# Kernel optimization log

Hardware: AMD Instinct MI355X
Metric: run time of the kernel (lower is better)

The kernel has to match this reference:

```python
import jax, jax.numpy as jnp
import numpy as np

N_NODES = 50000
N_EDGES = 800000
D = 128
SAME_W = 0.3
CROSS_W = 1.0


def setup_inputs() -> dict:
    key = jax.random.key(0)
    k1, k2, k3, k4, k5 = jax.random.split(key, 5)
    x = jax.random.normal(k1, (N_NODES, D), dtype=jnp.float32)
    edge_index = jax.random.randint(k2, (2, N_EDGES), 0, N_NODES, dtype=jnp.int64)
    edge_weight = jax.random.uniform(k3, (N_EDGES,), dtype=jnp.float32)
    Wr1 = jax.random.normal(k4, (D, D), dtype=jnp.float32) * (1.0 / np.sqrt(D))
    Wr2 = jax.random.normal(k5, (D, D), dtype=jnp.float32) * (1.0 / np.sqrt(D))
    return {"x": x, "edge_index": edge_index, "edge_weight": edge_weight,
            "Wr1": Wr1, "Wr2": Wr2, "cell_len": 20000}


def _node_types(idx, cell_len):
    # get_node_types: type 0 if idx <= cell_len, else 1 (note the <=, faithful to source)
    return (idx > cell_len).astype(jnp.int32)


def _conv_layer(x, src, dst, per_edge_w, Wr, n_nodes):
    # gather -> weight -> scatter-mean -> + root linear
    msg = x[src] * per_edge_w[:, None]                       # [E, D]
    agg = jax.ops.segment_sum(msg, dst, num_segments=n_nodes)  # [N, D]
    cnt = jax.ops.segment_sum(jnp.ones_like(per_edge_w), dst, num_segments=n_nodes)
    agg = agg / jnp.maximum(cnt, 1.0)[:, None]               # mean aggr (0 if no edges)
    return agg + x @ Wr.T                                     # lin_r, bias=False


def reference(x, edge_index, edge_weight, Wr1, Wr2, cell_len):
    src, dst = edge_index[0], edge_index[1]
    same = _node_types(src, cell_len) == _node_types(dst, cell_len)
    type_w = jnp.where(same, SAME_W, CROSS_W).astype(x.dtype)
    w = type_w * edge_weight                                  # [E]
    n_nodes = x.shape[0]
    h = _conv_layer(x, src, dst, w, Wr1, n_nodes)
    out = _conv_layer(h, src, dst, w, Wr2, n_nodes)
    return out
```

## Files before the change

kernel.cpp:

```cpp
#include <hip/hip_runtime.h>
#include <cstdint>
#include <cstddef>

#define D 128
#define SAME_W 0.3f
#define CROSS_W 1.0f
#define NSLICE 8
#define EPT 8
#define CAP 64
#define GEMM_BLOCKS 512

using bf16x8 = __attribute__((ext_vector_type(8))) __bf16;
using f32x4  = __attribute__((ext_vector_type(4))) float;

__device__ __forceinline__ unsigned bf16rne(float f) {
    unsigned u = __float_as_uint(f);
    return (u + 0x7FFFu + ((u >> 16) & 1u)) >> 16;
}

__global__ __launch_bounds__(256) void k_pre(
    const int* __restrict__ src, const int* __restrict__ dst,
    const float* __restrict__ ew, const int* __restrict__ cell_len,
    int* __restrict__ cnt, unsigned* __restrict__ meta, int E, int sliceLen,
    int nFill,
    const float4* __restrict__ x4, uint2* __restrict__ xh2,
    uint2* __restrict__ xl2, unsigned* __restrict__ xq, int nvec, int nSplit,
    const float* __restrict__ W1, const float* __restrict__ W2,
    unsigned* __restrict__ wsh, unsigned* __restrict__ w12h,
    unsigned* __restrict__ w12l)
{
    const int b = blockIdx.x;
    if (b < nFill) {
        const int slice = b & (NSLICE - 1);
        const int lo = slice * sliceLen, hi = lo + sliceLen;
        const int base = (b >> 3) * (256 * EPT) + threadIdx.x;
        const int c = *cell_len;
        #pragma unroll
        for (int u = 0; u < EPT; ++u) {
            int e = base + u * 256;
            if (e < E) {
                int d = __builtin_nontemporal_load(&dst[e]);
                if (d >= lo && d < hi) {
                    int s = __builtin_nontemporal_load(&src[e]);
                    float w = __builtin_nontemporal_load(&ew[e]);
                    float wt = w * (((s > c) == (d > c)) ? SAME_W : CROSS_W);
                    int pos = atomicAdd(&cnt[d], 1);
                    if (pos < CAP)
                        meta[d * CAP + pos] = (unsigned)s | (bf16rne(wt) << 16);
                }
            }
        }
    } else if (b < nFill + nSplit) {
        int i = (b - nFill) * 256 + threadIdx.x;
        if (i >= nvec) return;
        float4 v = x4[i];
        unsigned h0 = bf16rne(v.x), h1 = bf16rne(v.y),
                 h2 = bf16rne(v.z), h3 = bf16rne(v.w);
        xh2[i] = make_uint2(h0 | (h1 << 16), h2 | (h3 << 16));
        float r0 = v.x - __uint_as_float(h0 << 16);
        float r1 = v.y - __uint_as_float(h1 << 16);
        float r2 = v.z - __uint_as_float(h2 << 16);
        float r3 = v.w - __uint_as_float(h3 << 16);
        xl2[i] = make_uint2(bf16rne(r0) | (bf16rne(r1) << 16),
                            bf16rne(r2) | (bf16rne(r3) << 16));
        int q = __builtin_amdgcn_cvt_pk_fp8_f32(v.x, v.y, 0, false);
        q = __builtin_amdgcn_cvt_pk_fp8_f32(v.z, v.w, q, true);
        xq[i] = (unsigned)q;
    } else {
        int t = (b - nFill - nSplit) * 256 + threadIdx.x;
        int j = t >> 6, kp = t & 63;
        int k0 = kp * 2;
        float d0 = 0.f, d1 = 0.f;
        #pragma unroll 4
        for (int m = 0; m < D; ++m) {
            float a = W2[j * D + m];
            d0 = fmaf(a, W1[m * D + k0], d0);
            d1 = fmaf(a, W1[m * D + k0 + 1], d1);
        }
        float s0 = W1[j * D + k0] + W2[j * D + k0];
        float s1 = W1[j * D + k0 + 1] + W2[j * D + k0 + 1];
        wsh[j * 64 + kp] = bf16rne(s0) | (bf16rne(s1) << 16);
        unsigned h0 = bf16rne(d0), h1 = bf16rne(d1);
        w12h[j * 64 + kp] = h0 | (h1 << 16);
        float r0 = d0 - __uint_as_float(h0 << 16);
        float r1 = d1 - __uint_as_float(h1 << 16);
        w12l[j * 64 + kp] = bf16rne(r0) | (bf16rne(r1) << 16);
    }
}

template <bool EMIT_FP8>
__global__ __launch_bounds__(256) void k_agg_fp8(const unsigned short* __restrict__ xq,
                                                 const uint4* __restrict__ meta4,
                                                 const int* __restrict__ cnt,
                                                 unsigned* __restrict__ outb,
                                                 unsigned short* __restrict__ outq,
                                                 int N) {
    int gid = blockIdx.x * blockDim.x + threadIdx.x;
    int node = gid >> 6;
    int lane = gid & 63;
    if (node >= N) return;
    const int cn0 = cnt[node];
    const int cn = min(cn0, CAP);
    const uint4* mrow = meta4 + (size_t)node * (CAP / 4);
    float ax0 = 0.f, ay0 = 0.f, ax1 = 0.f, ay1 = 0.f;
    int i = 0;
    #pragma unroll 1
    for (; i + 16 <= cn; i += 16) {
        uint4 mq[4];
        #pragma unroll
        for (int u = 0; u < 4; ++u) mq[u] = mrow[(i >> 2) + u];
        unsigned short v[16];
        #pragma unroll
        for (int u = 0; u < 16; ++u) {
            unsigned m = ((const unsigned*)mq)[u];
            v[u] = xq[(size_t)(m & 0xFFFFu) * 64 + lane];
        }
        #pragma unroll
        for (int u = 0; u < 16; ++u) {
            unsigned m = ((const unsigned*)mq)[u];
            float wt = __uint_as_float(m & 0xFFFF0000u);
            float vx = __builtin_amdgcn_cvt_f32_fp8((unsigned)v[u], 0);
            float vy = __builtin_amdgcn_cvt_f32_fp8((unsigned)v[u], 1);
            if (u & 1) { ax1 = fmaf(vx, wt, ax1); ay1 = fmaf(vy, wt, ay1); }
            else       { ax0 = fmaf(vx, wt, ax0); ay0 = fmaf(vy, wt, ay0); }
        }
    }
    #pragma unroll 1
    for (; i + 4 <= cn; i += 4) {
        uint4 mq = mrow[i >> 2];
        unsigned short v[4];
        #pragma unroll
        for (int u = 0; u < 4; ++u)
            v[u] = xq[(size_t)(((const unsigned*)&mq)[u] & 0xFFFFu) * 64 + lane];
        #pragma unroll
        for (int u = 0; u < 4; ++u) {
            unsigned m = ((const unsigned*)&mq)[u];
            float wt = __uint_as_float(m & 0xFFFF0000u);
            float vx = __builtin_amdgcn_cvt_f32_fp8((unsigned)v[u], 0);
            float vy = __builtin_amdgcn_cvt_f32_fp8((unsigned)v[u], 1);
            if (u & 1) { ax1 = fmaf(vx, wt, ax1); ay1 = fmaf(vy, wt, ay1); }
            else       { ax0 = fmaf(vx, wt, ax0); ay0 = fmaf(vy, wt, ay0); }
        }
    }
    for (; i < cn; ++i) {
        unsigned m = ((const unsigned*)mrow)[i];
        float wt = __uint_as_float(m & 0xFFFF0000u);
        unsigned short v = xq[(size_t)(m & 0xFFFFu) * 64 + lane];
        ax0 = fmaf(__builtin_amdgcn_cvt_f32_fp8((unsigned)v, 0), wt, ax0);
        ay0 = fmaf(__builtin_amdgcn_cvt_f32_fp8((unsigned)v, 1), wt, ay0);
    }
    const float scale = 1.0f / (float)max(cn0, 1);
    const float rx = (ax0 + ax1) * scale, ry = (ay0 + ay1) * scale;
    outb[(size_t)node * 64 + lane] = bf16rne(rx) | (bf16rne(ry) << 16);
    if (EMIT_FP8) {
        int q = __builtin_amdgcn_cvt_pk_fp8_f32(rx, ry, 0, false);
        outq[(size_t)node * 64 + lane] = (unsigned short)(q & 0xFFFF);
    }
}

__global__ __launch_bounds__(256, 2) void k_gemm2(
    const uint4* __restrict__ xh4, const uint4* __restrict__ xl4,
    const uint4* __restrict__ a1h4,
    const uint4* __restrict__ w12h4, const uint4* __restrict__ w12l4,
    const uint4* __restrict__ wsh4,
    const unsigned* __restrict__ a2b,
    float* __restrict__ fout, int N, int nTiles)
{
    const int t = threadIdx.x;
    const int wave = t >> 6, lane = t & 63;
    const int j0 = wave * 32;
    const int lr = lane & 15;
    const int q  = lane >> 4;

    union FU { uint4 u; bf16x8 v; };

    FU wA[2][4], wB[2][4], wC[2][4];
    #pragma unroll
    for (int jt = 0; jt < 2; ++jt) {
        const int brow = (j0 + jt * 16 + lr) * 16 + q;
        #pragma unroll
        for (int ks = 0; ks < 4; ++ks) {
            wA[jt][ks].u = w12h4[brow + ks * 4];
            wB[jt][ks].u = w12l4[brow + ks * 4];
            wC[jt][ks].u = wsh4[brow + ks * 4];
        }
    }

#define LOAD_TILE(BX, BL, BA, BC, TILE) do {                                   \
    int row_ = (TILE) * 16 + lr; if (row_ > N - 1) row_ = N - 1;               \
    const int ar_ = row_ * 16 + q;                                             \
    _Pragma("unroll")                                                          \
    for (int ks = 0; ks < 4; ++ks) {                                           \
        BX[ks].u = xh4[ar_ + ks * 4];                                          \
        BL[ks].u = xl4[ar_ + ks * 4];                                          \
        BA[ks].u = a1h4[ar_ + ks * 4];                                         \
    }                                                                          \
    _Pragma("unroll")                                                          \
    for (int jt = 0; jt < 2; ++jt)                                             \
        _Pragma("unroll")                                                      \
        for (int r = 0; r < 4; ++r) {                                          \
            int rr_ = (TILE) * 16 + q * 4 + r; if (rr_ > N - 1) rr_ = N - 1;   \
            BC[jt * 4 + r] = a2b[(size_t)rr_ * 64 + ((j0 + jt * 16 + lr) >> 1)]; \
        }                                                                      \
} while (0)

#define COMPUTE_STORE(BX, BL, BA, BC, TILE) do {                               \
    f32x4 c_[2];                                                               \
    c_[0] = (f32x4){0.f, 0.f, 0.f, 0.f};                                       \
    c_[1] = (f32x4){0.f, 0.f, 0.f, 0.f};                                       \
    _Pragma("unroll")                                                          \
    for (int jt = 0; jt < 2; ++jt)                                             \
        _Pragma("unroll")                                                      \
        for (int ks = 0; ks < 4; ++ks) {                                       \
            c_[jt] = __builtin_amdgcn_mfma_f32_16x16x32_bf16(BX[ks].v, wA[jt][ks].v, c_[jt], 0, 0, 0); \
            c_[jt] = __builtin_amdgcn_mfma_f32_16x16x32_bf16(BL[ks].v, wA[jt][ks].v, c_[jt], 0, 0, 0); \
            c_[jt] = __builtin_amdgcn_mfma_f32_16x16x32_bf16(BX[ks].v, wB[jt][ks].v, c_[jt], 0, 0, 0); \
            c_[jt] = __builtin_amdgcn_mfma_f32_16x16x32_bf16(BA[ks].v, wC[jt][ks].v, c_[jt], 0, 0, 0); \
        }                                                                      \
    _Pragma("unroll")                                                          \
    for (int jt = 0; jt < 2; ++jt)                                             \
        _Pragma("unroll")                                                      \
        for (int r = 0; r < 4; ++r) {                                          \
            int rr_ = (TILE) * 16 + q * 4 + r;                                 \
            if (rr_ < N) {                                                     \
                unsigned w_ = BC[jt * 4 + r];                                  \
                float ci_ = __uint_as_float((lr & 1) ? (w_ & 0xFFFF0000u) : (w_ << 16)); \
                fout[(size_t)rr_ * D + j0 + jt * 16 + lr] = c_[jt][r] + ci_;   \
            }                                                                  \
        }                                                                      \
} while (0)

    FU Axh[4], Axl[4], Aa1[4]; unsigned Aci[8];
    FU Bxh[4], Bxl[4], Ba1[4]; unsigned Bci[8];

    int tile = blockIdx.x;
    const int step = gridDim.x;
    if (tile >= nTiles) return;
    LOAD_TILE(Axh, Axl, Aa1, Aci, tile);
    while (true) {
        int tn = tile + step;
        if (tn < nTiles) LOAD_TILE(Bxh, Bxl, Ba1, Bci, tn);
        COMPUTE_STORE(Axh, Axl, Aa1, Aci, tile);
        tile = tn;
        if (tile >= nTiles) break;
        tn = tile + step;
        if (tn < nTiles) LOAD_TILE(Axh, Axl, Aa1, Aci, tn);
        COMPUTE_STORE(Bxh, Bxl, Ba1, Bci, tile);
        tile = tn;
        if (tile >= nTiles) break;
    }
#undef LOAD_TILE
#undef COMPUTE_STORE
}

extern "C" void kernel_launch(void* const* d_in, const int* in_sizes, int n_in,
                              void* d_out, int out_size, void* d_ws, size_t ws_size,
                              hipStream_t stream) {
    const float* x        = (const float*)d_in[0];
    const int*   ei       = (const int*)d_in[1];
    const float* ew       = (const float*)d_in[2];
    const float* Wr1      = (const float*)d_in[3];
    const float* Wr2      = (const float*)d_in[4];
    const int*   cell_len = (const int*)d_in[5];

    const int N = in_sizes[0] / D;
    const int E = in_sizes[1] / 2;
    const int* src = ei;
    const int* dst = ei + E;

    char* ws = (char*)d_ws;
    size_t off = 0;
    unsigned* meta = (unsigned*)(ws + off); off += (size_t)4 * CAP * N;
    int*      cnt  = (int*)     (ws + off); off += (size_t)4 * N;
    off = (off + 255) & ~(size_t)255;
    unsigned* xh   = (unsigned*)(ws + off); off += (size_t)2 * N * D;
    unsigned* xl   = (unsigned*)(ws + off); off += (size_t)2 * N * D;
    unsigned* a1h  = (unsigned*)(ws + off); off += (size_t)2 * N * D;
    unsigned* a2b  = (unsigned*)(ws + off); off += (size_t)2 * N * D;
    unsigned* xq   = (unsigned*)(ws + off); off += (size_t)1 * N * D;
    unsigned* a1q  = (unsigned*)(ws + off); off += (size_t)1 * N * D;
    unsigned* wsh  = (unsigned*)(ws + off); off += (size_t)2 * D * D;
    unsigned* w12h = (unsigned*)(ws + off); off += (size_t)2 * D * D;
    unsigned* w12l = (unsigned*)(ws + off); off += (size_t)2 * D * D;
    if (ws_size < off) return;
    float* out = (float*)d_out;

    hipMemsetAsync(cnt, 0, (size_t)4 * N, stream);

    const int sliceLen = (N + NSLICE - 1) / NSLICE;
    const int nFill  = ((E + 256 * EPT - 1) / (256 * EPT)) * NSLICE;
    const int xvec   = N * D / 4;
    const int nSplit = (xvec + 255) / 256;
    const int nW     = (D * 64 + 255) / 256;
    const int aggBlocks = (N + 3) / 4;
    const int nTiles = (N + 15) / 16;

    k_pre<<<nFill + nSplit + nW, 256, 0, stream>>>(
        src, dst, ew, cell_len, cnt, meta, E, sliceLen, nFill,
        (const float4*)x, (uint2*)xh, (uint2*)xl, xq, xvec, nSplit,
        Wr1, Wr2, wsh, w12h, w12l);

    k_agg_fp8<true ><<<aggBlocks, 256, 0, stream>>>(
        (const unsigned short*)xq, (const uint4*)meta, cnt,
        a1h, (unsigned short*)a1q, N);
    k_agg_fp8<false><<<aggBlocks, 256, 0, stream>>>(
        (const unsigned short*)a1q, (const uint4*)meta, cnt,
        a2b, nullptr, N);

    k_gemm2<<<GEMM_BLOCKS, 256, 0, stream>>>((const uint4*)xh, (const uint4*)xl,
                                             (const uint4*)a1h,
                                             (const uint4*)w12h, (const uint4*)w12l,
                                             (const uint4*)wsh, a2b, out, N, nTiles);
}
```

Measured before the change: 224.4 us.

## Split x to bf16 hi/lo inside GEMM instead of materializing in preprocessing

```diff
diff --git a/kernel.cpp b/kernel.cpp
--- a/kernel.cpp
+++ b/kernel.cpp
@@ -6,16 +6,39 @@
 #define SAME_W 0.3f
 #define CROSS_W 1.0f
 #define NSLICE 8
-#define EPT 8
 #define CAP 64
 #define GEMM_BLOCKS 512
 
 using bf16x8 = __attribute__((ext_vector_type(8))) __bf16;
 using f32x4  = __attribute__((ext_vector_type(4))) float;
+using i32x4  = __attribute__((ext_vector_type(4))) int;
+using u32x4  = __attribute__((ext_vector_type(4))) unsigned;
 
 __device__ __forceinline__ unsigned bf16rne(float f) {
     unsigned u = __float_as_uint(f);
     return (u + 0x7FFFu + ((u >> 16) & 1u)) >> 16;
+}
+
+__device__ __forceinline__ void cvt8(const float4 a, const float4 b,
+                                     uint4& hi, uint4& lo) {
+    unsigned h0 = bf16rne(a.x), h1 = bf16rne(a.y),
+             h2 = bf16rne(a.z), h3 = bf16rne(a.w);
+    unsigned h4 = bf16rne(b.x), h5 = bf16rne(b.y),
+             h6 = bf16rne(b.z), h7 = bf16rne(b.w);
+    hi.x = h0 | (h1 << 16); hi.y = h2 | (h3 << 16);
+    hi.z = h4 | (h5 << 16); hi.w = h6 | (h7 << 16);
+    float r0 = a.x - __uint_as_float(h0 << 16);
+    float r1 = a.y - __uint_as_float(h1 << 16);
+    float r2 = a.z - __uint_as_float(h2 << 16);
+    float r3 = a.w - __uint_as_float(h3 << 16);
+    float r4 = b.x - __uint_as_float(h4 << 16);
+    float r5 = b.y - __uint_as_float(h5 << 16);
+    float r6 = b.z - __uint_as_float(h6 << 16);
+    float r7 = b.w - __uint_as_float(h7 << 16);
+    lo.x = bf16rne(r0) | (bf16rne(r1) << 16);
+    lo.y = bf16rne(r2) | (bf16rne(r3) << 16);
+    lo.z = bf16rne(r4) | (bf16rne(r5) << 16);
+    lo.w = bf16rne(r6) | (bf16rne(r7) << 16);
 }
 
 __global__ __launch_bounds__(256) void k_pre(
@@ -23,8 +46,7 @@
     const float* __restrict__ ew, const int* __restrict__ cell_len,
     int* __restrict__ cnt, unsigned* __restrict__ meta, int E, int sliceLen,
     int nFill,
-    const float4* __restrict__ x4, uint2* __restrict__ xh2,
-    uint2* __restrict__ xl2, unsigned* __restrict__ xq, int nvec, int nSplit,
+    const float* __restrict__ xf, u32x4* __restrict__ xq4, int nq, int nSplit,
     const float* __restrict__ W1, const float* __restrict__ W2,
     unsigned* __restrict__ wsh, unsigned* __restrict__ w12h,
     unsigned* __restrict__ w12l)
@@ -33,39 +55,65 @@
     if (b < nFill) {
         const int slice = b & (NSLICE - 1);
         const int lo = slice * sliceLen, hi = lo + sliceLen;
-        const int base = (b >> 3) * (256 * EPT) + threadIdx.x;
+        const int chunk = b >> 3;
         const int c = *cell_len;
         #pragma unroll
-        for (int u = 0; u < EPT; ++u) {
-            int e = base + u * 256;
-            if (e < E) {
-                int d = __builtin_nontemporal_load(&dst[e]);
-                if (d >= lo && d < hi) {
-                    int s = __builtin_nontemporal_load(&src[e]);
-                    float w = __builtin_nontemporal_load(&ew[e]);
-                    float wt = w * (((s > c) == (d > c)) ? SAME_W : CROSS_W);
-                    int pos = atomicAdd(&cnt[d], 1);
-                    if (pos < CAP)
-                        meta[d * CAP + pos] = (unsigned)s | (bf16rne(wt) << 16);
+        for (int u = 0; u < 2; ++u) {
+            const int e = chunk * 2048 + u * 1024 + (int)threadIdx.x * 4;
+            if (e + 3 < E) {
+                i32x4 d4 = __builtin_nontemporal_load((const i32x4*)(dst + e));
+                i32x4 s4 = __builtin_nontemporal_load((const i32x4*)(src + e));
+                f32x4 w4 = __builtin_nontemporal_load((const f32x4*)(ew + e));
+                #pragma unroll
+                for (int k = 0; k < 4; ++k) {
+                    const int d = d4[k];
+                    if (d >= lo && d < hi) {
+                        const int   s = s4[k];
+                        const float w = w4[k];
+                        float wt = w * (((s > c) == (d > c)) ? SAME_W : CROSS_W);
+                        int pos = atomicAdd(&cnt[d], 1);
+                        if (pos < CAP)
+                            meta[d * CAP + pos] = (unsigned)s | (bf16rne(wt) << 16);
+                    }
+                }
+            } else {
+                for (int k = 0; k < 4; ++k) {
+                    const int ee = e + k;
+                    if (ee < E) {
+                        int d = __builtin_nontemporal_load(&dst[ee]);
+                        if (d >= lo && d < hi) {
+                            int s = __builtin_nontemporal_load(&src[ee]);
+                            float w = __builtin_nontemporal_load(&ew[ee]);
+                            float wt = w * (((s > c) == (d > c)) ? SAME_W : CROSS_W);
+                            int pos = atomicAdd(&cnt[d], 1);
+                            if (pos < CAP)
+                                meta[d * CAP + pos] = (unsigned)s | (bf16rne(wt) << 16);
+                        }
+                    }
                 }
             }
         }
     } else if (b < nFill + nSplit) {
-        int i = (b - nFill) * 256 + threadIdx.x;
-        if (i >= nvec) return;
-        float4 v = x4[i];
-        unsigned h0 = bf16rne(v.x), h1 = bf16rne(v.y),
-                 h2 = bf16rne(v.z), h3 = bf16rne(v.w);
-        xh2[i] = make_uint2(h0 | (h1 << 16), h2 | (h3 << 16));
-        float r0 = v.x - __uint_as_float(h0 << 16);
-        float r1 = v.y - __uint_as_float(h1 << 16);
-        float r2 = v.z - __uint_as_float(h2 << 16);
-        float r3 = v.w - __uint_as_float(h3 << 16);
-        xl2[i] = make_uint2(bf16rne(r0) | (bf16rne(r1) << 16),
-                            bf16rne(r2) | (bf16rne(r3) << 16));
-        int q = __builtin_amdgcn_cvt_pk_fp8_f32(v.x, v.y, 0, false);
-        q = __builtin_amdgcn_cvt_pk_fp8_f32(v.z, v.w, q, true);
-        xq[i] = (unsigned)q;
+        int i = (b - nFill) * 256 + (int)threadIdx.x;
+        if (i >= nq) return;
+        const f32x4* px = (const f32x4*)(xf + (size_t)i * 16);
+        f32x4 v0 = __builtin_nontemporal_load(px);
+        f32x4 v1 = __builtin_nontemporal_load(px + 1);
+        f32x4 v2 = __builtin_nontemporal_load(px + 2);
+        f32x4 v3 = __builtin_nontemporal_load(px + 3);
+        u32x4 q;
+        {
+            int t;
+            t = __builtin_amdgcn_cvt_pk_fp8_f32(v0[0], v0[1], 0, false);
+            t = __builtin_amdgcn_cvt_pk_fp8_f32(v0[2], v0[3], t, true);  q[0] = (unsigned)t;
+            t = __builtin_amdgcn_cvt_pk_fp8_f32(v1[0], v1[1], 0, false);
+            t = __builtin_amdgcn_cvt_pk_fp8_f32(v1[2], v1[3], t, true);  q[1] = (unsigned)t;
+            t = __builtin_amdgcn_cvt_pk_fp8_f32(v2[0], v2[1], 0, false);
+            t = __builtin_amdgcn_cvt_pk_fp8_f32(v2[2], v2[3], t, true);  q[2] = (unsigned)t;
+            t = __builtin_amdgcn_cvt_pk_fp8_f32(v3[0], v3[1], 0, false);
+            t = __builtin_amdgcn_cvt_pk_fp8_f32(v3[2], v3[3], t, true);  q[3] = (unsigned)t;
+        }
+        xq4[i] = q;
     } else {
         int t = (b - nFill - nSplit) * 256 + threadIdx.x;
         int j = t >> 6, kp = t & 63;
@@ -159,7 +207,7 @@
 }
 
 __global__ __launch_bounds__(256, 2) void k_gemm2(
-    const uint4* __restrict__ xh4, const uint4* __restrict__ xl4,
+    const float4* __restrict__ xf,
     const uint4* __restrict__ a1h4,
     const uint4* __restrict__ w12h4, const uint4* __restrict__ w12l4,
     const uint4* __restrict__ wsh4,
@@ -186,13 +234,14 @@
         }
     }
 
-#define LOAD_TILE(BX, BL, BA, BC, TILE) do {                                   \
+#define LOAD_TILE(BXF, BA, BC, TILE) do {                                      \
     int row_ = (TILE) * 16 + lr; if (row_ > N - 1) row_ = N - 1;               \
     const int ar_ = row_ * 16 + q;                                             \
+    const int xr_ = row_ * 32 + q * 2;                                         \
     _Pragma("unroll")                                                          \
     for (int ks = 0; ks < 4; ++ks) {                                           \
-        BX[ks].u = xh4[ar_ + ks * 4];                                          \
-        BL[ks].u = xl4[ar_ + ks * 4];                                          \
+        BXF[2 * ks]     = xf[xr_ + ks * 8];                                    \
+        BXF[2 * ks + 1] = xf[xr_ + ks * 8 + 1];                                \
         BA[ks].u = a1h4[ar_ + ks * 4];                                         \
     }                                                                          \
     _Pragma("unroll")                                                          \
@@ -204,19 +253,22 @@
         }                                                                      \
 } while (0)
 
-#define COMPUTE_STORE(BX, BL, BA, BC, TILE) do {                               \
+#define COMPUTE_STORE(BXF, BA, BC, TILE) do {                                  \
     f32x4 c_[2];                                                               \
     c_[0] = (f32x4){0.f, 0.f, 0.f, 0.f};                                       \
     c_[1] = (f32x4){0.f, 0.f, 0.f, 0.f};                                       \
     _Pragma("unroll")                                                          \
-    for (int jt = 0; jt < 2; ++jt)                                             \
+    for (int ks = 0; ks < 4; ++ks) {                                           \
+        FU xh_, xl_;                                                           \
+        cvt8(BXF[2 * ks], BXF[2 * ks + 1], xh_.u, xl_.u);                      \
         _Pragma("unroll")                                                      \
-        for (int ks = 0; ks < 4; ++ks) {                                       \
-            c_[jt] = __builtin_amdgcn_mfma_f32_16x16x32_bf16(BX[ks].v, wA[jt][ks].v, c_[jt], 0, 0, 0); \
-            c_[jt] = __builtin_amdgcn_mfma_f32_16x16x32_bf16(BL[ks].v, wA[jt][ks].v, c_[jt], 0, 0, 0); \
-            c_[jt] = __builtin_amdgcn_mfma_f32_16x16x32_bf16(BX[ks].v, wB[jt][ks].v, c_[jt], 0, 0, 0); \
+        for (int jt = 0; jt < 2; ++jt) {                                       \
+            c_[jt] = __builtin_amdgcn_mfma_f32_16x16x32_bf16(xh_.v, wA[jt][ks].v, c_[jt], 0, 0, 0); \
+            c_[jt] = __builtin_amdgcn_mfma_f32_16x16x32_bf16(xl_.v, wA[jt][ks].v, c_[jt], 0, 0, 0); \
+            c_[jt] = __builtin_amdgcn_mfma_f32_16x16x32_bf16(xh_.v, wB[jt][ks].v, c_[jt], 0, 0, 0); \
             c_[jt] = __builtin_amdgcn_mfma_f32_16x16x32_bf16(BA[ks].v, wC[jt][ks].v, c_[jt], 0, 0, 0); \
         }                                                                      \
+    }                                                                          \
     _Pragma("unroll")                                                          \
     for (int jt = 0; jt < 2; ++jt)                                             \
         _Pragma("unroll")                                                      \
@@ -230,22 +282,22 @@
         }                                                                      \
 } while (0)
 
-    FU Axh[4], Axl[4], Aa1[4]; unsigned Aci[8];
-    FU Bxh[4], Bxl[4], Ba1[4]; unsigned Bci[8];
+    float4 Axf[8]; FU Aa1[4]; unsigned Aci[8];
+    float4 Bxf[8]; FU Ba1[4]; unsigned Bci[8];
 
     int tile = blockIdx.x;
     const int step = gridDim.x;
     if (tile >= nTiles) return;
-    LOAD_TILE(Axh, Axl, Aa1, Aci, tile);
+    LOAD_TILE(Axf, Aa1, Aci, tile);
     while (true) {
         int tn = tile + step;
-        if (tn < nTiles) LOAD_TILE(Bxh, Bxl, Ba1, Bci, tn);
-        COMPUTE_STORE(Axh, Axl, Aa1, Aci, tile);
+        if (tn < nTiles) LOAD_TILE(Bxf, Ba1, Bci, tn);
+        COMPUTE_STORE(Axf, Aa1, Aci, tile);
         tile = tn;
         if (tile >= nTiles) break;
         tn = tile + step;
-        if (tn < nTiles) LOAD_TILE(Axh, Axl, Aa1, Aci, tn);
-        COMPUTE_STORE(Bxh, Bxl, Ba1, Bci, tile);
+        if (tn < nTiles) LOAD_TILE(Axf, Aa1, Aci, tn);
+        COMPUTE_STORE(Bxf, Ba1, Bci, tile);
         tile = tn;
         if (tile >= nTiles) break;
     }
@@ -273,8 +325,6 @@
     unsigned* meta = (unsigned*)(ws + off); off += (size_t)4 * CAP * N;
     int*      cnt  = (int*)     (ws + off); off += (size_t)4 * N;
     off = (off + 255) & ~(size_t)255;
-    unsigned* xh   = (unsigned*)(ws + off); off += (size_t)2 * N * D;
-    unsigned* xl   = (unsigned*)(ws + off); off += (size_t)2 * N * D;
     unsigned* a1h  = (unsigned*)(ws + off); off += (size_t)2 * N * D;
     unsigned* a2b  = (unsigned*)(ws + off); off += (size_t)2 * N * D;
     unsigned* xq   = (unsigned*)(ws + off); off += (size_t)1 * N * D;
@@ -288,16 +338,16 @@
     hipMemsetAsync(cnt, 0, (size_t)4 * N, stream);
 
     const int sliceLen = (N + NSLICE - 1) / NSLICE;
-    const int nFill  = ((E + 256 * EPT - 1) / (256 * EPT)) * NSLICE;
-    const int xvec   = N * D / 4;
-    const int nSplit = (xvec + 255) / 256;
+    const int nFill  = ((E + 2047) / 2048) * NSLICE;
+    const int nq     = N * D / 16;
+    const int nSplit = (nq + 255) / 256;
     const int nW     = (D * 64 + 255) / 256;
     const int aggBlocks = (N + 3) / 4;
     const int nTiles = (N + 15) / 16;
 
     k_pre<<<nFill + nSplit + nW, 256, 0, stream>>>(
         src, dst, ew, cell_len, cnt, meta, E, sliceLen, nFill,
-        (const float4*)x, (uint2*)xh, (uint2*)xl, xq, xvec, nSplit,
+        x, (u32x4*)xq, nq, nSplit,
         Wr1, Wr2, wsh, w12h, w12l);
 
     k_agg_fp8<true ><<<aggBlocks, 256, 0, stream>>>(
@@ -307,7 +357,7 @@
         (const unsigned short*)a1q, (const uint4*)meta, cnt,
         a2b, nullptr, N);
 
-    k_gemm2<<<GEMM_BLOCKS, 256, 0, stream>>>((const uint4*)xh, (const uint4*)xl,
+    k_gemm2<<<GEMM_BLOCKS, 256, 0, stream>>>((const float4*)x,
                                              (const uint4*)a1h,
                                              (const uint4*)w12h, (const uint4*)w12l,
                                              (const uint4*)wsh, a2b, out, N, nTiles);
```

New measurement: 251.8 us. 12.2% more time.
